# Kernel optimization log

Measured on AMD Instinct MI355X. Metric: run time of the kernel, lower is better.

The kernel has to match this reference:

```python
import jax, jax.numpy as jnp
import numpy as np

B, N, H, C = 64, 307, 64, 12   # batch, nodes, hidden_channels, input_channels
D = H * C                       # GATv2 out_channels = hidden*input
E = 2456                        # number of (random) graph edges
NEG_SLOPE = 0.2


def setup_inputs() -> dict:
    key = jax.random.key(0)
    ks = jax.random.split(key, 8)
    sW = 1.0 / np.sqrt(H)
    sA = 1.0 / np.sqrt(D)
    return {
        "t": 0,
        "z": jax.random.normal(ks[0], (B * N, H), jnp.float32),
        "r1": jax.random.randint(ks[1], (E,), 0, N),
        "r2": jax.random.randint(ks[2], (E,), 0, N),
        "Wl": (jax.random.normal(ks[3], (H, D), jnp.float32) * sW),
        "bl": jnp.zeros((D,), jnp.float32),
        "Wr": (jax.random.normal(ks[4], (H, D), jnp.float32) * sW),
        "br": jnp.zeros((D,), jnp.float32),
        "att": (jax.random.normal(ks[5], (D,), jnp.float32) * sA),
        "bias": jnp.zeros((D,), jnp.float32),
    }


def _gatv2_batched(x, src, dst, Wl, bl, Wr, br, att, bias):
    # x: [B, N, H]; identical topology for all batch samples, so the
    # per-sample Python loop in the original collapses to one batched pass.
    xl = jnp.einsum("bnh,hd->nbd", x, Wl) + bl  # [N, B, D]  (lin_l, messages)
    xr = jnp.einsum("bnh,hd->nbd", x, Wr) + br  # [N, B, D]  (lin_r, targets)
    h = xl[src] + xr[dst]                        # [E+N, B, D]
    e = jnp.einsum("ebd,d->eb", jax.nn.leaky_relu(h, NEG_SLOPE), att)  # [E+N, B]
    # edge softmax over incoming edges of each target node (dst)
    emax = jax.ops.segment_max(e, dst, num_segments=N)   # [N, B]
    ee = jnp.exp(e - emax[dst])
    denom = jax.ops.segment_sum(ee, dst, num_segments=N)  # [N, B]
    alpha = ee / denom[dst]                                # [E+N, B]
    out = jax.ops.segment_sum(alpha[:, :, None] * xl[src], dst, num_segments=N)
    return out + bias                                      # [N, B, D]


def reference(t, z, r1, r2, Wl, bl, Wr, br, att, bias):
    x = z.reshape(B, N, H)
    # PyG GATv2Conv with add_self_loops=True: append one self loop per node.
    loops = jnp.arange(N)
    src = jnp.concatenate([r1, loops])
    dst = jnp.concatenate([r2, loops])
    out = _gatv2_batched(x, src, dst, Wl, bl, Wr, br, att, bias)  # [N, B, D]
    out = out.transpose(1, 0, 2)          # [B, N, D]
    return out.reshape(B * N, H, C)
```

## Files before the change

kernel.cpp:

```cpp
#include <hip/hip_runtime.h>

#define BB 64
#define NN 307
#define HH 64
#define DD 768
#define EE 2456
#define ET 2763
#define MM (BB*NN)
#define DEGMAX 128
#define SEGCAP 48
#define NG 77

#define XL_OFF   0u
#define XL_SZ    (MM*DD*2u)
#define XR_OFF   (XL_OFF + XL_SZ)
#define GSRC_OFF (XR_OFF + XL_SZ)
#define GDEG_OFF (GSRC_OFF + NN*DEGMAX*4u)

typedef __attribute__((ext_vector_type(8))) _Float16 half8;
typedef __attribute__((ext_vector_type(2))) _Float16 h2;
typedef __attribute__((ext_vector_type(4))) float f32x4;
typedef __attribute__((ext_vector_type(2))) float f32x2;
typedef __attribute__((ext_vector_type(4))) unsigned u32x4;
typedef __attribute__((ext_vector_type(2))) unsigned u32x2;

#if defined(__has_builtin)
#if __has_builtin(__builtin_amdgcn_fdot2)
#define HAS_FDOT2 1
#endif
#endif

__device__ __forceinline__ unsigned short f2h(float f){
  union{_Float16 h; unsigned short u;} c; c.h = (_Float16)f; return c.u;
}
__device__ __forceinline__ h2 u2h(unsigned u){
  union{unsigned u; h2 h;} c; c.u = u; return c.h;
}

__global__ __launch_bounds__(256) void k_gemm(
    const float* __restrict__ z,
    const float* __restrict__ Wl, const float* __restrict__ bl,
    const float* __restrict__ Wr, const float* __restrict__ br,
    const int* __restrict__ r1, const int* __restrict__ r2,
    int* __restrict__ gdeg, int* __restrict__ gsrc,
    unsigned short* __restrict__ xl, unsigned short* __restrict__ xr)
{
  __shared__ unsigned short sBTl[128][72];
  __shared__ unsigned short sBTr[128][72];
  __shared__ unsigned short sC[64][136];
  __shared__ int sseg[4][SEGCAP];
  __shared__ int scnt[4];

  const int tid = threadIdx.x;
  const int lane = tid & 63, wv = tid >> 6;

  if (blockIdx.z == 1){
    if (blockIdx.y != 0) return;
    const int n = blockIdx.x;
    const int W = (ET + 3) / 4;
    const int e0 = wv * W;
    const int e1 = (e0 + W < ET) ? e0 + W : ET;
    int cnt = 0;
    for (int base = e0; base < e1; base += 64){
      int e = base + lane;
      int d = -1, s = 0;
      if (e < e1){
        if (e < EE){ d = r2[e]; s = r1[e]; }
        else       { d = e - EE; s = d; }
      }
      bool hit = (d == n);
      unsigned long long mb = __ballot(hit);
      if (hit){
        int pos = cnt + (int)__popcll(mb & ((1ull << lane) - 1ull));
        if (pos < SEGCAP) sseg[wv][pos] = s;
      }
      cnt += (int)__popcll(mb);
    }
    if (lane == 0) scnt[wv] = (cnt < SEGCAP) ? cnt : SEGCAP;
    __syncthreads();
    int c0 = scnt[0], c1 = scnt[1], c2 = scnt[2], c3 = scnt[3];
    int off = (wv > 0 ? c0 : 0) + (wv > 1 ? c1 : 0) + (wv > 2 ? c2 : 0);
    int cw = scnt[wv];
    int deg = c0 + c1 + c2 + c3;
    if (lane < cw && off + lane < DEGMAX) gsrc[n*DEGMAX + off + lane] = sseg[wv][lane];
    if (tid == 0) gdeg[n] = (deg < DEGMAX) ? deg : DEGMAX;
    return;
  }

  const int m0 = blockIdx.x*64, n0 = blockIdx.y*128;

  #pragma unroll
  for (int it=0; it<32; it++){
    int idx = it*256 + tid;
    int k = idx >> 7, c = idx & 127;
    sBTl[c][k] = f2h(Wl[(size_t)k*DD + n0 + c]);
    sBTr[c][k] = f2h(Wr[(size_t)k*DD + n0 + c]);
  }

  const int arow = m0 + wv*16 + (lane & 15);
  const int kp   = (lane >> 4) * 8;
  const float* pz = z + (size_t)arow*HH + kp;
  float4 za0 = *(const float4*)(pz);
  float4 za1 = *(const float4*)(pz + 4);
  float4 zb0 = *(const float4*)(pz + 32);
  float4 zb1 = *(const float4*)(pz + 36);
  half8 a0, a1;
  a0[0]=(_Float16)za0.x; a0[1]=(_Float16)za0.y; a0[2]=(_Float16)za0.z; a0[3]=(_Float16)za0.w;
  a0[4]=(_Float16)za1.x; a0[5]=(_Float16)za1.y; a0[6]=(_Float16)za1.z; a0[7]=(_Float16)za1.w;
  a1[0]=(_Float16)zb0.x; a1[1]=(_Float16)zb0.y; a1[2]=(_Float16)zb0.z; a1[3]=(_Float16)zb0.w;
  a1[4]=(_Float16)zb1.x; a1[5]=(_Float16)zb1.y; a1[6]=(_Float16)zb1.z; a1[7]=(_Float16)zb1.w;
  __syncthreads();

  const int bcol = lane & 15;
  f32x4 accl[8], accr[8];
  #pragma unroll
  for (int cb=0; cb<8; cb++){
    accl[cb][0]=0.f; accl[cb][1]=0.f; accl[cb][2]=0.f; accl[cb][3]=0.f;
    accr[cb][0]=0.f; accr[cb][1]=0.f; accr[cb][2]=0.f; accr[cb][3]=0.f;
  }

  #pragma unroll
  for (int cb=0; cb<8; cb++){
    half8 b0l = *(const half8*)&sBTl[cb*16 + bcol][kp];
    half8 b1l = *(const half8*)&sBTl[cb*16 + bcol][32 + kp];
    accl[cb] = __builtin_amdgcn_mfma_f32_16x16x32_f16(a0, b0l, accl[cb], 0, 0, 0);
    accl[cb] = __builtin_amdgcn_mfma_f32_16x16x32_f16(a1, b1l, accl[cb], 0, 0, 0);
    half8 b0r = *(const half8*)&sBTr[cb*16 + bcol][kp];
    half8 b1r = *(const half8*)&sBTr[cb*16 + bcol][32 + kp];
    accr[cb] = __builtin_amdgcn_mfma_f32_16x16x32_f16(a0, b0r, accr[cb], 0, 0, 0);
    accr[cb] = __builtin_amdgcn_mfma_f32_16x16x32_f16(a1, b1r, accr[cb], 0, 0, 0);
  }

  #pragma unroll
  for (int cb=0; cb<8; cb++){
    int cc = cb*16 + bcol;
    float bb = bl[n0 + cc];
    #pragma unroll
    for (int r=0; r<4; r++){
      int rr = wv*16 + (lane>>4)*4 + r;
      sC[rr][cc] = f2h(accl[cb][r] + bb);
    }
  }
  __syncthreads();
  #pragma unroll
  for (int it=0; it<4; it++){
    int idx = it*256 + tid;
    int rr = idx >> 4;
    int c8 = (idx & 15) * 8;
    uint4 v = *(const uint4*)&sC[rr][c8];
    *(uint4*)&xl[(size_t)(m0+rr)*DD + n0 + c8] = v;
  }
  __syncthreads();
  #pragma unroll
  for (int cb=0; cb<8; cb++){
    int cc = cb*16 + bcol;
    float bb = br[n0 + cc];
    #pragma unroll
    for (int r=0; r<4; r++){
      int rr = wv*16 + (lane>>4)*4 + r;
      sC[rr][cc] = f2h(accr[cb][r] + bb);
    }
  }
  __syncthreads();
  #pragma unroll
  for (int it=0; it<4; it++){
    int idx = it*256 + tid;
    int rr = idx >> 4;
    int c8 = (idx & 15) * 8;
    uint4 v = *(const uint4*)&sC[rr][c8];
    *(uint4*)&xr[(size_t)(m0+rr)*DD + n0 + c8] = v;
  }
}


template<int CTRL, int RM>
__device__ __forceinline__ float dpp_add(float v){
  int x = __builtin_amdgcn_update_dpp(0, __float_as_int(v), CTRL, RM, 0xf, true);
  return v + __int_as_float(x);
}
__device__ __forceinline__ float redux64s(float v){
  v = dpp_add<0x121,0xf>(v);
  v = dpp_add<0x122,0xf>(v);
  v = dpp_add<0x124,0xf>(v);
  v = dpp_add<0x128,0xf>(v);
  v = dpp_add<0x142,0xa>(v);
  v = dpp_add<0x143,0x8>(v);
  return __uint_as_float((unsigned)__builtin_amdgcn_readlane(__float_as_int(v), 63));
}

#define LOAD6(DST, P) {                                           \
  u32x4 _u0 = *(const u32x4*)((P) + duA);                         \
  u32x2 _u1 = *(const u32x2*)((P) + duB);                         \
  DST[0]=_u0.x; DST[1]=_u0.y; DST[2]=_u0.z; DST[3]=_u0.w;         \
  DST[4]=_u1.x; DST[5]=_u1.y; }

#define READS(J) __builtin_amdgcn_readlane((((J) & 64) ? sv1 : sv0), (J) & 63)
#define EADDR(J)  ((const unsigned*)(xlb + (size_t)READS(J)*DD))
#define EADDRC(J) ({ int _q = (J); int _qc = _q < degm1 ? _q : degm1;  \
                     (const unsigned*)(xlb + (size_t)READS(_qc)*DD); })

#define MKH(H, U) {                                               \
  _Pragma("unroll")                                               \
  for (int _t=0;_t<6;_t++) H[_t] = u2h(U[_t]) + xrh[_t]; }

#ifdef HAS_FDOT2
#define SCORE(S, H) {                                             \
  _Pragma("unroll")                                               \
  for (int _t=0;_t<6;_t++){                                       \
    h2 _l = __builtin_elementwise_max(H[_t], H[_t]*c02h);         \
    S = __builtin_amdgcn_fdot2(_l, atth[_t], S, false); } }
#else
#define SCORE(S, H) {                                             \
  _Pragma("unroll")                                               \
  for (int _t=0;_t<6;_t++){                                       \
    h2 _l = __builtin_elementwise_max(H[_t], H[_t]*c02h);         \
    S += (float)_l[0]*attf[2*_t] + (float)_l[1]*attf[2*_t+1]; } }
#endif

#define ACCH(P, H) {                                              \
  _Pragma("unroll")                                               \
  for (int _t=0;_t<6;_t++){                                       \
    acc2[_t].x += (P) * (float)H[_t][0];                          \
    acc2[_t].y += (P) * (float)H[_t][1]; } }

#define STEP2(U, V) {                                             \
  h2 hU[6], hV[6];                                                \
  MKH(hU, U); MKH(hV, V);                                         \
  float sU = 0.f, sV = 0.f;                                       \
  SCORE(sU, hU); SCORE(sV, hV);                                   \
  float scU = redux64s(sU);                                       \
  float scV = redux64s(sV);                                       \
  float pU = __builtin_amdgcn_exp2f(scU - C2);                    \
  float pV = __builtin_amdgcn_exp2f(scV - C2);                    \
  ssum += pU + pV;                                                \
  ACCH(pU, hU); ACCH(pV, hV); }

#define STEP1(U) {                                                \
  h2 hU[6];                                                       \
  MKH(hU, U);                                                     \
  float sU = 0.f;                                                 \
  SCORE(sU, hU);                                                  \
  float scU = redux64s(sU);                                       \
  float pU = __builtin_amdgcn_exp2f(scU - C2);                    \
  ssum += pU;                                                     \
  ACCH(pU, hU); }

__global__ __launch_bounds__(256) void k_fusedf(
    const unsigned short* __restrict__ xl, const unsigned short* __restrict__ xr,
    const int* __restrict__ gdeg, const int* __restrict__ gsrc,
    const float* __restrict__ att, const float* __restrict__ bias,
    float* __restrict__ out)
{
  const unsigned id = blockIdx.x;
  const int xcd = (int)(id & 7u);
  const unsigned k = id >> 3;
  const int b = xcd + 8 * (int)(k / NG);
  const int g = (int)(k % NG);
  const int wv = threadIdx.x >> 6;
  const int nv = g*4 + wv;
  if (nv >= NN) return;
  const int n = __builtin_amdgcn_readfirstlane(nv);
  const int lane = threadIdx.x & 63;
  const int duA = lane * 4;
  const int duB = 256 + lane * 2;

  int sv0 = gsrc[n*DEGMAX + lane];
  int sv1 = gsrc[n*DEGMAX + 64 + lane];
  const int deg = __builtin_amdgcn_readfirstlane(gdeg[n]);
  const int degm1 = deg - 1;

  f32x2 ar[6];
  {
    const f32x2* paA = (const f32x2*)(att) + lane*4;
    const f32x2* paB = (const f32x2*)(att + 512) + lane*2;
    #pragma unroll
    for (int t=0;t<4;t++) ar[t] = paA[t];
    #pragma unroll
    for (int t=0;t<2;t++) ar[4+t] = paB[t];
  }
  const unsigned* px = (const unsigned*)(xr + ((size_t)b*NN + n)*DD);
  u32x4 x0 = __builtin_nontemporal_load((const u32x4*)(px + duA));
  u32x2 x1 = __builtin_nontemporal_load((const u32x2*)(px + duB));

  const unsigned short* xlb = xl + (size_t)b*NN*DD;

  unsigned bA[6], bB[6], bC[6], bD[6], bE[6], bF[6];
  LOAD6(bA, EADDR(0));
  LOAD6(bB, EADDRC(1));
  LOAD6(bC, EADDRC(2));
  LOAD6(bD, EADDRC(3));
  LOAD6(bE, EADDRC(4));
  LOAD6(bF, EADDRC(5));

  h2 atth[6], xrh[6];
  const h2 c02h = {(_Float16)0.2f, (_Float16)0.2f};
#ifndef HAS_FDOT2
  float attf[12];
#endif
  #pragma unroll
  for (int t=0;t<6;t++){
    atth[t][0] = (_Float16)(ar[t].x * 1.4426950408889634f);
    atth[t][1] = (_Float16)(ar[t].y * 1.4426950408889634f);
#ifndef HAS_FDOT2
    attf[2*t]   = ar[t].x * 1.4426950408889634f;
    attf[2*t+1] = ar[t].y * 1.4426950408889634f;
#endif
  }
  {
    unsigned xx[6] = {x0.x, x0.y, x0.z, x0.w, x1.x, x1.y};
    #pragma unroll
    for (int t=0;t<6;t++) xrh[t] = u2h(xx[t]);
  }
  f32x2 acc2[6];
  #pragma unroll
  for (int t=0;t<6;t++){ acc2[t].x = 0.f; acc2[t].y = 0.f; }

  float ssum = 0.f;
  const float C2 = 11.5415603f;

  int i = 0;
  for (; i + 6 <= deg; ){
    const bool more = (i + 6 < deg);
    STEP2(bA, bB);
    if (more){ LOAD6(bA, EADDRC(i+6));  LOAD6(bB, EADDRC(i+7));  }
    STEP2(bC, bD);
    if (more){ LOAD6(bC, EADDRC(i+8));  LOAD6(bD, EADDRC(i+9));  }
    STEP2(bE, bF);
    if (more){ LOAD6(bE, EADDRC(i+10)); LOAD6(bF, EADDRC(i+11)); }
    i += 6;
  }
  {
    const int rem = deg - i;
    if (rem >= 2){ STEP2(bA, bB); } else if (rem == 1){ STEP1(bA); }
    if (rem >= 4){ STEP2(bC, bD); } else if (rem == 3){ STEP1(bC); }
    if (rem == 5){ STEP1(bE); }
  }

  const float inv = 1.f / ssum;
  float* po = out + ((size_t)b*NN + n)*DD;
  const f32x2* pbA = (const f32x2*)(bias) + lane*4;
  const f32x2* pbB = (const f32x2*)(bias + 512) + lane*2;
  f32x2 pb[6];
  #pragma unroll
  for (int t=0;t<4;t++) pb[t] = pbA[t];
  #pragma unroll
  for (int t=0;t<2;t++) pb[4+t] = pbB[t];

  f32x2 o2[6];
  #pragma unroll
  for (int t=0;t<6;t++){
    o2[t].x = acc2[t].x * inv + (pb[t].x - (float)xrh[t][0]);
    o2[t].y = acc2[t].y * inv + (pb[t].y - (float)xrh[t][1]);
  }
  {
    f32x4 oa; oa[0]=o2[0].x; oa[1]=o2[0].y; oa[2]=o2[1].x; oa[3]=o2[1].y;
    f32x4 ob; ob[0]=o2[2].x; ob[1]=o2[2].y; ob[2]=o2[3].x; ob[3]=o2[3].y;
    f32x4 oc; oc[0]=o2[4].x; oc[1]=o2[4].y; oc[2]=o2[5].x; oc[3]=o2[5].y;
    __builtin_nontemporal_store(oa, (f32x4*)(po + lane*8));
    __builtin_nontemporal_store(ob, (f32x4*)(po + lane*8 + 4));
    __builtin_nontemporal_store(oc, (f32x4*)(po + 512 + lane*4));
  }
}

extern "C" void kernel_launch(void* const* d_in, const int* in_sizes, int n_in,
                              void* d_out, int out_size, void* d_ws, size_t ws_size,
                              hipStream_t stream)
{
  const float* z   = (const float*)d_in[1];
  const int*   r1  = (const int*)  d_in[2];
  const int*   r2  = (const int*)  d_in[3];
  const float* Wl  = (const float*)d_in[4];
  const float* bl  = (const float*)d_in[5];
  const float* Wr  = (const float*)d_in[6];
  const float* br  = (const float*)d_in[7];
  const float* att = (const float*)d_in[8];
  const float* bias= (const float*)d_in[9];
  float* out = (float*)d_out;

  char* ws = (char*)d_ws;
  unsigned short* xl = (unsigned short*)(ws + XL_OFF);
  unsigned short* xr = (unsigned short*)(ws + XR_OFF);
  int* gsrc = (int*)(ws + GSRC_OFF);
  int* gdeg = (int*)(ws + GDEG_OFF);

  k_gemm<<<dim3(MM/64, DD/128, 2), 256, 0, stream>>>(z, Wl, bl, Wr, br,
                                                     r1, r2, gdeg, gsrc, xl, xr);
  k_fusedf<<<dim3(8*8*NG, 1, 1), 256, 0, stream>>>(xl, xr, gdeg, gsrc, att, bias, out);
}
```

Before: 63.44 us.

## Split each node's incoming edges across four waves and reduce via shared memory

Each block now handles one (batch, node) pair, and its four wavefronts take interleaved subsets of that node's incoming edges. Previously one wave walked all edges of a node. The partial accumulators and exp-sums are combined through LDS after a block barrier, and wave 0 writes the output. This is meant to shorten the serial per-node dependency chain and expose more parallelism per node. In exchange it launches four times as many blocks, adds LDS traffic and a __syncthreads, drops the 6-deep load prefetch to 2-deep, and makes every wave redundantly load att and xr.

```diff
diff --git a/kernel.cpp b/kernel.cpp
--- a/kernel.cpp
+++ b/kernel.cpp
@@ -9,7 +9,6 @@
 #define MM (BB*NN)
 #define DEGMAX 128
 #define SEGCAP 48
-#define NG 77
 
 #define XL_OFF   0u
 #define XL_SZ    (MM*DD*2u)
@@ -196,8 +195,6 @@
 
 #define READS(J) __builtin_amdgcn_readlane((((J) & 64) ? sv1 : sv0), (J) & 63)
 #define EADDR(J)  ((const unsigned*)(xlb + (size_t)READS(J)*DD))
-#define EADDRC(J) ({ int _q = (J); int _qc = _q < degm1 ? _q : degm1;  \
-                     (const unsigned*)(xlb + (size_t)READS(_qc)*DD); })
 
 #define MKH(H, U) {                                               \
   _Pragma("unroll")                                               \
@@ -223,21 +220,10 @@
     acc2[_t].x += (P) * (float)H[_t][0];                          \
     acc2[_t].y += (P) * (float)H[_t][1]; } }
 
-#define STEP2(U, V) {                                             \
-  h2 hU[6], hV[6];                                                \
-  MKH(hU, U); MKH(hV, V);                                         \
-  float sU = 0.f, sV = 0.f;                                       \
-  SCORE(sU, hU); SCORE(sV, hV);                                   \
-  float scU = redux64s(sU);                                       \
-  float scV = redux64s(sV);                                       \
-  float pU = __builtin_amdgcn_exp2f(scU - C2);                    \
-  float pV = __builtin_amdgcn_exp2f(scV - C2);                    \
-  ssum += pU + pV;                                                \
-  ACCH(pU, hU); ACCH(pV, hV); }
-
-#define STEP1(U) {                                                \
+#define STEP1R(U, C, JN) {                                        \
   h2 hU[6];                                                       \
   MKH(hU, U);                                                     \
+  if (C) LOAD6(U, EADDR(JN));                                     \
   float sU = 0.f;                                                 \
   SCORE(sU, hU);                                                  \
   float scU = redux64s(sU);                                       \
@@ -252,22 +238,21 @@
     float* __restrict__ out)
 {
   const unsigned id = blockIdx.x;
-  const int xcd = (int)(id & 7u);
-  const unsigned k = id >> 3;
-  const int b = xcd + 8 * (int)(k / NG);
-  const int g = (int)(k % NG);
+  const unsigned kk = id >> 3;
+  const int bhi = (int)(kk / NN);
+  const int n   = (int)(kk % NN);
+  const int b   = (int)(id & 7u) + 8*bhi;
   const int wv = threadIdx.x >> 6;
-  const int nv = g*4 + wv;
-  if (nv >= NN) return;
-  const int n = __builtin_amdgcn_readfirstlane(nv);
   const int lane = threadIdx.x & 63;
   const int duA = lane * 4;
   const int duB = 256 + lane * 2;
 
+  __shared__ float sAcc[3][64][26];
+
   int sv0 = gsrc[n*DEGMAX + lane];
   int sv1 = gsrc[n*DEGMAX + 64 + lane];
   const int deg = __builtin_amdgcn_readfirstlane(gdeg[n]);
-  const int degm1 = deg - 1;
+  const int cw = (deg - wv + 3) >> 2;
 
   f32x2 ar[6];
   {
@@ -279,18 +264,14 @@
     for (int t=0;t<2;t++) ar[4+t] = paB[t];
   }
   const unsigned* px = (const unsigned*)(xr + ((size_t)b*NN + n)*DD);
-  u32x4 x0 = __builtin_nontemporal_load((const u32x4*)(px + duA));
-  u32x2 x1 = __builtin_nontemporal_load((const u32x2*)(px + duB));
+  u32x4 x0 = *(const u32x4*)(px + duA);
+  u32x2 x1 = *(const u32x2*)(px + duB);
 
   const unsigned short* xlb = xl + (size_t)b*NN*DD;
 
-  unsigned bA[6], bB[6], bC[6], bD[6], bE[6], bF[6];
-  LOAD6(bA, EADDR(0));
-  LOAD6(bB, EADDRC(1));
-  LOAD6(bC, EADDRC(2));
-  LOAD6(bD, EADDRC(3));
-  LOAD6(bE, EADDRC(4));
-  LOAD6(bF, EADDRC(5));
+  unsigned uA[6], uB[6];
+  if (cw >= 1) LOAD6(uA, EADDR(wv));
+  if (cw >= 2) LOAD6(uB, EADDR(wv + 4));
 
   h2 atth[6], xrh[6];
   const h2 c02h = {(_Float16)0.2f, (_Float16)0.2f};
@@ -319,21 +300,29 @@
   const float C2 = 11.5415603f;
 
   int i = 0;
-  for (; i + 6 <= deg; ){
-    const bool more = (i + 6 < deg);
-    STEP2(bA, bB);
-    if (more){ LOAD6(bA, EADDRC(i+6));  LOAD6(bB, EADDRC(i+7));  }
-    STEP2(bC, bD);
-    if (more){ LOAD6(bC, EADDRC(i+8));  LOAD6(bD, EADDRC(i+9));  }
-    STEP2(bE, bF);
-    if (more){ LOAD6(bE, EADDRC(i+10)); LOAD6(bF, EADDRC(i+11)); }
-    i += 6;
-  }
-  {
-    const int rem = deg - i;
-    if (rem >= 2){ STEP2(bA, bB); } else if (rem == 1){ STEP1(bA); }
-    if (rem >= 4){ STEP2(bC, bD); } else if (rem == 3){ STEP1(bC); }
-    if (rem == 5){ STEP1(bE); }
+  for (; i + 2 <= cw; i += 2){
+    STEP1R(uA, (i + 2 < cw), wv + 4*(i+2));
+    STEP1R(uB, (i + 3 < cw), wv + 4*(i+3));
+  }
+  if (i < cw) STEP1R(uA, false, 0);
+
+  if (wv > 0){
+    float* s = &sAcc[wv-1][lane][0];
+    #pragma unroll
+    for (int t=0;t<6;t++){ s[2*t] = acc2[t].x; s[2*t+1] = acc2[t].y; }
+    #pragma unroll
+    for (int t=0;t<6;t++){ }
+    s[24] = ssum;
+  }
+  __syncthreads();
+  if (wv != 0) return;
+
+  #pragma unroll
+  for (int w=0; w<3; w++){
+    const float* s = &sAcc[w][lane][0];
+    #pragma unroll
+    for (int t=0;t<6;t++){ acc2[t].x += s[2*t]; acc2[t].y += s[2*t+1]; }
+    ssum += s[24];
   }
 
   const float inv = 1.f / ssum;
@@ -385,5 +374,5 @@
 
   k_gemm<<<dim3(MM/64, DD/128, 2), 256, 0, stream>>>(z, Wl, bl, Wr, br,
                                                      r1, r2, gdeg, gsrc, xl, xr);
-  k_fusedf<<<dim3(8*8*NG, 1, 1), 256, 0, stream>>>(xl, xr, gdeg, gsrc, att, bias, out);
-}
+  k_fusedf<<<dim3(MM, 1, 1), 256, 0, stream>>>(xl, xr, gdeg, gsrc, att, bias, out);
+}
```

Measured after the change: 65.81 us. +3.7%, slower.
